# Optimization experiments

Measured on AMD Instinct MI355X. Metric: run time of the kernel, lower is better.

The kernel has to match this reference:

```python
import jax, jax.numpy as jnp
import numpy as np


def setup_inputs() -> dict:
    key = jax.random.key(0)
    k1, k2 = jax.random.split(key)
    B = 16384
    y_pred = jax.random.normal(k1, (B,), dtype=jnp.float32)
    y_true = jax.random.randint(k2, (B,), 0, 2, dtype=jnp.int64)
    return {"y_pred": y_pred, "y_true": y_true}


def reference(y_pred, y_true):
    # pos_pred[i] - neg_pred[j] over all (pos, neg) pairs, expressed with a
    # mask-weighted mean so shapes stay static under jit (same math as the
    # boolean-gather version when both classes are present).
    pos = (y_true == 1).astype(y_pred.dtype)  # [B]
    neg = (y_true == 0).astype(y_pred.dtype)  # [B]
    # pairwise_diff[i, j] = y_pred[i] - y_pred[j]
    diff = y_pred[:, None] - y_pred[None, :]  # [B, B]
    w = pos[:, None] * neg[None, :]           # [B, B] pair mask
    s = jax.nn.sigmoid(-diff)
    loss = jnp.sum(s * w) / jnp.sum(w)
    return loss
```

## Files before the change

kernel.cpp:

```cpp
#include <hip/hip_runtime.h>
#include <math.h>


#define NODES 2049
#define NPAD  2052
#define SLEN  4097
#define KC    8
#define HB    16

static constexpr float LO    = -12.0f;
static constexpr float DELTA = 24.0f / 2048.0f;
static constexpr float INVD  = 2048.0f / 24.0f;
static constexpr float LOG2E = 1.4426950408889634f;


__global__ __launch_bounds__(1024)
void hist_k(const float* __restrict__ pred, const int* __restrict__ yt, int B,
            float* __restrict__ g_h ,
            int* __restrict__ g_Pc ) {
    __shared__ float h[2 * NPAD];
    const int t = threadIdx.x;
    const int b = blockIdx.x;

    for (int i = t; i < 2 * NPAD; i += 1024) h[i] = 0.f;
    __syncthreads();

    int cp = 0;
    for (int e = b * 1024 + t; e < B; e += HB * 1024) {
        float p = pred[e];
        int   c = yt[e];
        float x = (p - LO) * INVD;
        x = fminf(fmaxf(x, 0.f), 2047.999f);
        int   k = (int)x;
        float f = x - (float)k;
        int base = (c == 1) ? 0 : NPAD;
        cp += (c == 1);
        atomicAdd(&h[base + k],     1.f - f);
        atomicAdd(&h[base + k + 1], f);
    }
    __syncthreads();

    float* dst = g_h + (size_t)b * 2 * NPAD;
    for (int i = t; i < NODES; i += 1024) {
        dst[i]        = h[i];
        dst[NPAD + i] = h[NPAD + i];
    }

    #pragma unroll
    for (int off = 32; off; off >>= 1) cp += __shfl_down(cp, off, 64);
    __shared__ int wc[16];
    if ((t & 63) == 0) wc[t >> 6] = cp;
    __syncthreads();
    if (t == 0) {
        int s = 0;
        #pragma unroll
        for (int k = 0; k < 16; ++k) s += wc[k];
        g_Pc[b] = s;
    }
}


__global__ __launch_bounds__(256)
void conv_k(const float* __restrict__ g_h, float* __restrict__ partial) {
    __shared__ float sS[SLEN];
    __shared__ float sN[NODES];
    const int t = threadIdx.x;
    const int bk = blockIdx.x;

    for (int i = t; i < NODES; i += 256) {
        float s = 0.f;
        #pragma unroll
        for (int b = 0; b < HB; ++b) s += g_h[(size_t)b * 2 * NPAD + NPAD + i];
        sN[i] = s;
    }
    for (int i = t; i < SLEN; i += 256) {
        float d = (float)(i - 2048) * DELTA;
        float e = __builtin_amdgcn_exp2f(d * LOG2E);
        sS[i] = __builtin_amdgcn_rcpf(1.f + e);
    }
    __syncthreads();

    float acc = 0.f;
    #pragma unroll
    for (int kk = 0; kk < KC; ++kk) {
        int k = bk * KC + kk;
        if (k < NODES) {
            float hPk = 0.f;
            #pragma unroll
            for (int b = 0; b < HB; ++b) hPk += g_h[(size_t)b * 2 * NPAD + k];
            if (hPk != 0.f) {
                const float* Sk = &sS[k + 2048];
                for (int l = t; l < NODES; l += 256)
                    acc += hPk * (sN[l] * Sk[-l]);
            }
        }
    }

    #pragma unroll
    for (int off = 32; off; off >>= 1) acc += __shfl_down(acc, off, 64);
    __shared__ float wa[4];
    if ((t & 63) == 0) wa[t >> 6] = acc;
    __syncthreads();
    if (t == 0) partial[bk] = (wa[0] + wa[1]) + (wa[2] + wa[3]);
}


__global__ __launch_bounds__(256)
void reduce_k(const float* __restrict__ partial, int nPart,
              const int* __restrict__ g_Pc, int B, float* __restrict__ out) {
    const int t = threadIdx.x;
    double s = 0.0;
    for (int i = t; i < nPart; i += 256) s += (double)partial[i];
    int cp = 0;
    if (t < HB) cp = g_Pc[t];
    #pragma unroll
    for (int off = 32; off; off >>= 1) {
        s  += __shfl_down(s, off, 64);
        cp += __shfl_down(cp, off, 64);
    }
    __shared__ double wa[4];
    __shared__ int    wp[4];
    if ((t & 63) == 0) { wa[t >> 6] = s; wp[t >> 6] = cp; }
    __syncthreads();
    if (t == 0) {
        double S = (wa[0] + wa[1]) + (wa[2] + wa[3]);
        double P = (double)(wp[0] + wp[1] + wp[2] + wp[3]);
        double N = (double)B - P;
        out[0] = (float)(S / (P * N));
    }
}

extern "C" void kernel_launch(void* const* d_in, const int* in_sizes, int n_in,
                              void* d_out, int out_size, void* d_ws, size_t ws_size,
                              hipStream_t stream) {
    const float* pred = (const float*)d_in[0];
    const int*   yt   = (const int*)d_in[1];
    const int B = in_sizes[0];
    float* out = (float*)d_out;

    float* g_h  = (float*)d_ws;
    int*   g_Pc = (int*)(g_h + (size_t)HB * 2 * NPAD);
    float* part = (float*)(g_Pc + 64);

    const int nBlk = (NODES + KC - 1) / KC;

    hist_k<<<HB, 1024, 0, stream>>>(pred, yt, B, g_h, g_Pc);
    conv_k<<<nBlk, 256, 0, stream>>>(g_h, part);
    reduce_k<<<1, 256, 0, stream>>>(part, nBlk, g_Pc, B, out);
}
```

Before: 72.08 us.

## Fuse histogram, convolution and reduction into one kernel with flag-based grid sync

```diff
diff --git a/kernel.cpp b/kernel.cpp
--- a/kernel.cpp
+++ b/kernel.cpp
@@ -6,88 +6,101 @@
 #define NPAD  2052
 #define SLEN  4097
 #define KC    8
-#define HB    16
+#define NB    257
+#define HB    8
+#define HWIN  2048
 
+static constexpr unsigned MAGIC = 0x13579BDFu;
 static constexpr float LO    = -12.0f;
 static constexpr float DELTA = 24.0f / 2048.0f;
 static constexpr float INVD  = 2048.0f / 24.0f;
 static constexpr float LOG2E = 1.4426950408889634f;
 
+__global__ __launch_bounds__(256)
+void fused_k(const float* __restrict__ pred, const int* __restrict__ yt, int B,
+             float* __restrict__ g_h ,
+             int* __restrict__ g_Pc, unsigned* __restrict__ hFlag,
+             float* __restrict__ partial, unsigned* __restrict__ cFlag,
+             float* __restrict__ out) {
+    __shared__ float sS[SLEN];
+    __shared__ float sN[NODES];
+    __shared__ float h[2 * NPAD];
+    __shared__ float wa[4];
+    __shared__ int   wc[4];
+    __shared__ double da[4];
 
-__global__ __launch_bounds__(1024)
-void hist_k(const float* __restrict__ pred, const int* __restrict__ yt, int B,
-            float* __restrict__ g_h ,
-            int* __restrict__ g_Pc ) {
-    __shared__ float h[2 * NPAD];
-    const int t = threadIdx.x;
-    const int b = blockIdx.x;
+    const int t    = threadIdx.x;
+    const int b    = blockIdx.x;
+    const int lane = t & 63;
+    const int w    = t >> 6;
 
-    for (int i = t; i < 2 * NPAD; i += 1024) h[i] = 0.f;
-    __syncthreads();
+    for (int i = t; i < SLEN; i += 256) {
+        float d = (float)(i - 2048) * DELTA;
+        float e = __builtin_amdgcn_exp2f(d * LOG2E);
+        sS[i] = __builtin_amdgcn_rcpf(1.f + e);
+    }
 
-    int cp = 0;
-    for (int e = b * 1024 + t; e < B; e += HB * 1024) {
-        float p = pred[e];
-        int   c = yt[e];
-        float x = (p - LO) * INVD;
-        x = fminf(fmaxf(x, 0.f), 2047.999f);
-        int   k = (int)x;
-        float f = x - (float)k;
-        int base = (c == 1) ? 0 : NPAD;
-        cp += (c == 1);
-        atomicAdd(&h[base + k],     1.f - f);
-        atomicAdd(&h[base + k + 1], f);
+    if (b < HB) {
+        for (int i = t; i < 2 * NPAD; i += 256) h[i] = 0.f;
+        __syncthreads();
+        int cp = 0;
+        for (int e0 = b * HWIN; e0 < B; e0 += HB * HWIN) {
+            int lim = min(e0 + HWIN, B);
+            for (int e = e0 + t; e < lim; e += 256) {
+                float p = pred[e];
+                int   c = yt[e];
+                float x = (p - LO) * INVD;
+                x = fminf(fmaxf(x, 0.f), 2047.999f);
+                int   k = (int)x;
+                float f = x - (float)k;
+                int base = (c == 1) ? 0 : NPAD;
+                cp += (c == 1);
+                atomicAdd(&h[base + k],     1.f - f);
+                atomicAdd(&h[base + k + 1], f);
+            }
+        }
+        __syncthreads();
+        float* dst = g_h + (size_t)b * (2 * NPAD);
+        for (int i = t; i < NODES; i += 256) {
+            dst[i]        = h[i];
+            dst[NPAD + i] = h[NPAD + i];
+        }
+        #pragma unroll
+        for (int off = 32; off; off >>= 1) cp += __shfl_down(cp, off, 64);
+        if (lane == 0) wc[w] = cp;
+        __syncthreads();
+        if (t == 0) {
+            g_Pc[b] = (wc[0] + wc[1]) + (wc[2] + wc[3]);
+            __threadfence();
+            __hip_atomic_store(&hFlag[b], MAGIC,
+                               __ATOMIC_RELEASE, __HIP_MEMORY_SCOPE_AGENT);
+        }
+    }
+
+    if (t == 0) {
+        for (int q = 0; q < HB; ++q)
+            while (__hip_atomic_load(&hFlag[q], __ATOMIC_ACQUIRE,
+                                     __HIP_MEMORY_SCOPE_AGENT) != MAGIC)
+                __builtin_amdgcn_s_sleep(1);
     }
     __syncthreads();
-
-    float* dst = g_h + (size_t)b * 2 * NPAD;
-    for (int i = t; i < NODES; i += 1024) {
-        dst[i]        = h[i];
-        dst[NPAD + i] = h[NPAD + i];
-    }
-
-    #pragma unroll
-    for (int off = 32; off; off >>= 1) cp += __shfl_down(cp, off, 64);
-    __shared__ int wc[16];
-    if ((t & 63) == 0) wc[t >> 6] = cp;
-    __syncthreads();
-    if (t == 0) {
-        int s = 0;
-        #pragma unroll
-        for (int k = 0; k < 16; ++k) s += wc[k];
-        g_Pc[b] = s;
-    }
-}
-
-
-__global__ __launch_bounds__(256)
-void conv_k(const float* __restrict__ g_h, float* __restrict__ partial) {
-    __shared__ float sS[SLEN];
-    __shared__ float sN[NODES];
-    const int t = threadIdx.x;
-    const int bk = blockIdx.x;
 
     for (int i = t; i < NODES; i += 256) {
         float s = 0.f;
         #pragma unroll
-        for (int b = 0; b < HB; ++b) s += g_h[(size_t)b * 2 * NPAD + NPAD + i];
+        for (int q = 0; q < HB; ++q) s += g_h[(size_t)q * (2 * NPAD) + NPAD + i];
         sN[i] = s;
-    }
-    for (int i = t; i < SLEN; i += 256) {
-        float d = (float)(i - 2048) * DELTA;
-        float e = __builtin_amdgcn_exp2f(d * LOG2E);
-        sS[i] = __builtin_amdgcn_rcpf(1.f + e);
     }
     __syncthreads();
 
     float acc = 0.f;
     #pragma unroll
     for (int kk = 0; kk < KC; ++kk) {
-        int k = bk * KC + kk;
+        int k = b * KC + kk;
         if (k < NODES) {
             float hPk = 0.f;
             #pragma unroll
-            for (int b = 0; b < HB; ++b) hPk += g_h[(size_t)b * 2 * NPAD + k];
+            for (int q = 0; q < HB; ++q) hPk += g_h[(size_t)q * (2 * NPAD) + k];
             if (hPk != 0.f) {
                 const float* Sk = &sS[k + 2048];
                 for (int l = t; l < NODES; l += 256)
@@ -95,38 +108,38 @@
             }
         }
     }
-
     #pragma unroll
     for (int off = 32; off; off >>= 1) acc += __shfl_down(acc, off, 64);
-    __shared__ float wa[4];
-    if ((t & 63) == 0) wa[t >> 6] = acc;
-    __syncthreads();
-    if (t == 0) partial[bk] = (wa[0] + wa[1]) + (wa[2] + wa[3]);
-}
-
-
-__global__ __launch_bounds__(256)
-void reduce_k(const float* __restrict__ partial, int nPart,
-              const int* __restrict__ g_Pc, int B, float* __restrict__ out) {
-    const int t = threadIdx.x;
-    double s = 0.0;
-    for (int i = t; i < nPart; i += 256) s += (double)partial[i];
-    int cp = 0;
-    if (t < HB) cp = g_Pc[t];
-    #pragma unroll
-    for (int off = 32; off; off >>= 1) {
-        s  += __shfl_down(s, off, 64);
-        cp += __shfl_down(cp, off, 64);
-    }
-    __shared__ double wa[4];
-    __shared__ int    wp[4];
-    if ((t & 63) == 0) { wa[t >> 6] = s; wp[t >> 6] = cp; }
+    if (lane == 0) wa[w] = acc;
     __syncthreads();
     if (t == 0) {
-        double S = (wa[0] + wa[1]) + (wa[2] + wa[3]);
-        double P = (double)(wp[0] + wp[1] + wp[2] + wp[3]);
-        double N = (double)B - P;
-        out[0] = (float)(S / (P * N));
+        partial[b] = (wa[0] + wa[1]) + (wa[2] + wa[3]);
+        __threadfence();
+        __hip_atomic_store(&cFlag[b], MAGIC,
+                           __ATOMIC_RELEASE, __HIP_MEMORY_SCOPE_AGENT);
+    }
+
+    if (b == 0) {
+        while (__hip_atomic_load(&cFlag[t + 1], __ATOMIC_ACQUIRE,
+                                 __HIP_MEMORY_SCOPE_AGENT) != MAGIC)
+            __builtin_amdgcn_s_sleep(1);
+        __syncthreads();
+        double s = 0.0;
+        for (int i = t; i < NB; i += 256) s += (double)partial[i];
+        int cp = (t < HB) ? g_Pc[t] : 0;
+        #pragma unroll
+        for (int off = 32; off; off >>= 1) {
+            s  += __shfl_down(s, off, 64);
+            cp += __shfl_down(cp, off, 64);
+        }
+        if (lane == 0) { da[w] = s; wc[w] = cp; }
+        __syncthreads();
+        if (t == 0) {
+            double S = (da[0] + da[1]) + (da[2] + da[3]);
+            double P = (double)((wc[0] + wc[1]) + (wc[2] + wc[3]));
+            double N = (double)B - P;
+            out[0] = (float)(S / (P * N));
+        }
     }
 }
 
@@ -138,13 +151,13 @@
     const int B = in_sizes[0];
     float* out = (float*)d_out;
 
-    float* g_h  = (float*)d_ws;
-    int*   g_Pc = (int*)(g_h + (size_t)HB * 2 * NPAD);
-    float* part = (float*)(g_Pc + 64);
+    char* ws = (char*)d_ws;
+    float*    g_h   = (float*)ws;
+    int*      g_Pc  = (int*)(g_h + (size_t)HB * 2 * NPAD);
+    unsigned* hFlag = (unsigned*)(g_Pc + 64);
+    float*    part  = (float*)(hFlag + 64);
+    unsigned* cFlag = (unsigned*)(part + ((NB + 63) & ~63));
 
-    const int nBlk = (NODES + KC - 1) / KC;
-
-    hist_k<<<HB, 1024, 0, stream>>>(pred, yt, B, g_h, g_Pc);
-    conv_k<<<nBlk, 256, 0, stream>>>(g_h, part);
-    reduce_k<<<1, 256, 0, stream>>>(part, nBlk, g_Pc, B, out);
+    fused_k<<<NB, 256, 0, stream>>>(pred, yt, B, g_h, g_Pc, hFlag,
+                                    part, cFlag, out);
 }
```

After: 108.9 us. 1.51x slower.
